# Optimization experiments

Hardware: AMD Instinct MI355X
Metric: run time of the kernel (lower is better)

Reference implementation:

```python
import jax, jax.numpy as jnp
import numpy as np

N = 100000   # nodes
E = 600000   # edges
D = 128      # in_dim == out_dim
ED = 6       # edge_dim
LN_EPS = 1e-5


def setup_inputs() -> dict:
    key = jax.random.key(0)
    ks = jax.random.split(key, 12)
    s = 1.0 / np.sqrt(D)
    se = 1.0 / np.sqrt(ED)
    return {
        "x": jax.random.normal(ks[0], (N, D), dtype=jnp.float32),
        "edge_index": jax.random.randint(ks[1], (2, E), 0, N, dtype=jnp.int64),
        "edge_attr": jax.random.normal(ks[2], (E, ED), dtype=jnp.float32),
        "batch": jnp.zeros((N,), dtype=jnp.int64),
        "W_e": jax.random.uniform(ks[3], (ED, D), jnp.float32, -se, se),
        "b_e": jax.random.uniform(ks[4], (D,), jnp.float32, -se, se),
        "eps": jnp.zeros((), dtype=jnp.float32),  # GINE train_eps init 0
        "W1": jax.random.uniform(ks[5], (D, D), jnp.float32, -s, s),
        "b1": jax.random.uniform(ks[6], (D,), jnp.float32, -s, s),
        "W2": jax.random.uniform(ks[7], (D, D), jnp.float32, -s, s),
        "b2": jax.random.uniform(ks[8], (D,), jnp.float32, -s, s),
        "gamma": jnp.ones((D,), dtype=jnp.float32),
        "beta": jnp.zeros((D,), dtype=jnp.float32),
    }


def reference(x, edge_index, edge_attr, batch, W_e, b_e, eps, W1, b1, W2, b2, gamma, beta):
    src, dst = edge_index[0], edge_index[1]
    # edge embedding: Linear(edge_dim -> in_dim)
    edge_emb = edge_attr @ W_e + b_e                      # [E, D]
    # GINEConv message: ReLU(x_j + edge_emb), scatter-add to target nodes
    msg = jax.nn.relu(x[src] + edge_emb)                  # [E, D]
    agg = jax.ops.segment_sum(msg, dst, num_segments=N)   # [N, D]
    h = (1.0 + eps) * x + agg                             # [N, D]
    # GINE nn: Linear -> ReLU -> Linear
    h = jax.nn.relu(h @ W1 + b1) @ W2 + b2                # [N, D]
    # LayerNorm over feature dim
    mu = jnp.mean(h, axis=-1, keepdims=True)
    var = jnp.var(h, axis=-1, keepdims=True)
    h = (h - mu) * jax.lax.rsqrt(var + LN_EPS) * gamma + beta
    # activation=True -> ReLU; dropout identity in eval mode
    return jax.nn.relu(h)
```

## Files before the change

### kernel.cpp

```cpp
#include <hip/hip_runtime.h>
#include <stdint.h>

#define NN 100000
#define EE 600000
#define DD 128

typedef _Float16 half8 __attribute__((ext_vector_type(8)));
typedef _Float16 h2 __attribute__((ext_vector_type(2)));
typedef float f32x4 __attribute__((ext_vector_type(4)));

static __device__ __forceinline__ uint32_t pack2(float a, float b) {
    h2 h; h.x = (_Float16)a; h.y = (_Float16)b;
    return __builtin_bit_cast(uint32_t, h);
}
static __device__ __forceinline__ h2 cvt22(float2 f) {
    h2 r; r.x = (_Float16)f.x; r.y = (_Float16)f.y; return r;
}

#define NB_HIST ((EE + 255) / 256)
#define NB_CONV (NN * DD / 4 / 256)
template<bool CONV>
__global__ __launch_bounds__(256)
void setup_kernel(const int* __restrict__ ei, const float* __restrict__ x,
                  const float* __restrict__ W1, const float* __restrict__ W2,
                  int* __restrict__ counts, uint32_t* __restrict__ xh,
                  _Float16* __restrict__ w1h, _Float16* __restrict__ w2h)
{
    const int nbc = CONV ? NB_CONV : 0;
    const int b = blockIdx.x, tid = threadIdx.x;
    if (b < NB_HIST) {
        int e = b * 256 + tid;
        if (e < EE) atomicAdd(&counts[ei[EE + e]], 1);
    } else if (CONV && b < NB_HIST + nbc) {
        int i = (b - NB_HIST) * 256 + tid;
        float4 v = ((const float4*)x)[i];
        uint2 o; o.x = pack2(v.x, v.y); o.y = pack2(v.z, v.w);
        ((uint2*)xh)[i] = o;
    } else {
        int t = (b - NB_HIST - nbc) * 256 + tid;
        if (t < 2 * DD * DD) {
            int which = t >> 14;
            int idx = t & (DD * DD - 1);
            int k = idx >> 7, d = idx & 127;
            float wv = (which ? W2 : W1)[k * DD + d];
            int kt = k >> 5, kr = k & 31;
            int grp = kr >> 3, j = kr & 7;
            int nt = d >> 4, cc = d & 15;
            int off = ((kt * 8 + nt) * 64 + grp * 16 + cc) * 8 + j;
            (which ? w2h : w1h)[off] = (_Float16)wv;
        }
    }
}

__global__ __launch_bounds__(256)
void scan_blocks(const int* __restrict__ counts, int* __restrict__ startv,
                 int* __restrict__ bsum)
{
    const int t = threadIdx.x;
    const int idx = blockIdx.x * 1024 + t * 4;
    int4 v = {0, 0, 0, 0};
    if (idx < NN) v = *(const int4*)(counts + idx);
    int s1 = v.x + v.y, s2 = s1 + v.z, s3 = s2 + v.w;
    const int lane = t & 63;
    int q = s3;
#pragma unroll
    for (int off = 1; off < 64; off <<= 1) {
        int u = __shfl_up(q, off, 64);
        if (lane >= off) q += u;
    }
    __shared__ int wsum[4];
    if (lane == 63) wsum[t >> 6] = q;
    __syncthreads();
    const int w = t >> 6;
    int pre = 0;
    if (w > 0) pre += wsum[0];
    if (w > 1) pre += wsum[1];
    if (w > 2) pre += wsum[2];
    const int excl = (q - s3) + pre;
    if (idx < NN) {
        int4 o = {excl, excl + v.x, excl + s1, excl + s2};
        *(int4*)(startv + idx) = o;
    }
    __syncthreads();
    if (t == 0) bsum[blockIdx.x] = wsum[0] + wsum[1] + wsum[2] + wsum[3];
}

__global__ __launch_bounds__(128)
void scan_top(const int* __restrict__ bsum, int* __restrict__ boff)
{
    __shared__ int sm[128];
    const int t = threadIdx.x;
    const int NB = (NN + 1023) / 1024;
    int v = (t < NB) ? bsum[t] : 0;
    sm[t] = v;
    __syncthreads();
#pragma unroll
    for (int off = 1; off < 128; off <<= 1) {
        int u = (t >= off) ? sm[t - off] : 0;
        __syncthreads();
        sm[t] += u;
        __syncthreads();
    }
    boff[t] = sm[t] - v;
}

__global__ __launch_bounds__(256)
void fixup_start(int* __restrict__ start, const int* __restrict__ boff)
{
    int i = blockIdx.x * 256 + threadIdx.x;
    if (i < NN) start[i] += boff[i >> 10];
    if (i == 0) start[NN] = EE;
}

__global__ __launch_bounds__(256)
void scatter_rec(const int* __restrict__ ei, const float* __restrict__ ea,
                 const int* __restrict__ start, int* __restrict__ cursor,
                 float* __restrict__ rec)
{
    int e = blockIdx.x * 256 + threadIdx.x;
    if (e >= EE) return;
    int dst = ei[EE + e];
    int src = ei[e];
    int pos = start[dst] + atomicAdd(&cursor[dst], 1);
    const float2* eap = (const float2*)(ea + e * 6);
    float2 e01 = eap[0];
    float2 e23 = eap[1];
    float2 e45 = eap[2];
    float4 r;
    r.x = __int_as_float(src);
    r.y = __uint_as_float(pack2(e01.x, e01.y));
    r.z = __uint_as_float(pack2(e23.x, e23.y));
    r.w = __uint_as_float(pack2(e45.x, e45.y));
    *(float4*)(rec + (size_t)pos * 4) = r;
}

#define NWAVE 8192
template<bool XH>
__global__ __launch_bounds__(256)
void agg_pk(const float* __restrict__ x, const uint32_t* __restrict__ xh,
            const float* __restrict__ rec, const float* __restrict__ We,
            const float* __restrict__ be, const int* __restrict__ start,
            const float* __restrict__ epsp, uint32_t* __restrict__ h0h)
{
    const int w = blockIdx.x * 4 + (threadIdx.x >> 6);
    const int lane = threadIdx.x & 63;
    const int d0 = lane * 2;
    const h2 w0h = cvt22(*(const float2*)(We + 0 * DD + d0));
    const h2 w1h = cvt22(*(const float2*)(We + 1 * DD + d0));
    const h2 w2h = cvt22(*(const float2*)(We + 2 * DD + d0));
    const h2 w3h = cvt22(*(const float2*)(We + 3 * DD + d0));
    const h2 w4h = cvt22(*(const float2*)(We + 4 * DD + d0));
    const h2 w5h = cvt22(*(const float2*)(We + 5 * DD + d0));
    const h2 bbh = cvt22(*(const float2*)(be + d0));
    h2 zero2; zero2.x = (_Float16)0.f; zero2.y = (_Float16)0.f;
    const float sc = 1.0f + epsp[0];
    const int n0 = (int)(((long long)w * NN) >> 13);
    const int n1 = (int)(((long long)(w + 1) * NN) >> 13);

#define EDGE_PK(R, XV, WGT) do {                                                \
        h2 c01 = __builtin_bit_cast(h2, (R).y);                                 \
        h2 c23 = __builtin_bit_cast(h2, (R).z);                                 \
        h2 c45 = __builtin_bit_cast(h2, (R).w);                                 \
        h2 emb = bbh, s;                                                        \
        s.x = c01.x; s.y = c01.x; emb = s * w0h + emb;                          \
        s.x = c01.y; s.y = c01.y; emb = s * w1h + emb;                          \
        s.x = c23.x; s.y = c23.x; emb = s * w2h + emb;                          \
        s.x = c23.y; s.y = c23.y; emb = s * w3h + emb;                          \
        s.x = c45.x; s.y = c45.x; emb = s * w4h + emb;                          \
        s.x = c45.y; s.y = c45.y; emb = s * w5h + emb;                          \
        h2 m = (XV) + emb;                                                      \
        m = __builtin_elementwise_max(m, zero2);                                \
        ax = fmaf((WGT), (float)m.x, ax);                                       \
        ay = fmaf((WGT), (float)m.y, ay);                                       \
    } while (0)

    for (int n = n0; n < n1; ++n) {
        const int begin = start[n];
        const int cnt = start[n + 1] - begin;
        const float4* rp = (const float4*)rec + begin;
        float ax = 0.f, ay = 0.f;
        for (int i = 0; i < cnt; i += 4) {
            const int rem = cnt - i;
            const int ia = i;
            const int ib = i + (rem > 1 ? 1 : 0);
            const int ic = i + (rem > 2 ? 2 : 0);
            const int id = i + (rem > 3 ? 3 : 0);
            float4 ra = rp[ia], rb = rp[ib], rc = rp[ic], rd = rp[id];
            int sa = __float_as_int(ra.x), sb = __float_as_int(rb.x),
                sc3 = __float_as_int(rc.x), sd = __float_as_int(rd.x);
            h2 xa, xb, xc, xd;
            if constexpr (XH) {
                xa = __builtin_bit_cast(h2, xh[((uint32_t)sa << 6) + lane]);
                xb = __builtin_bit_cast(h2, xh[((uint32_t)sb << 6) + lane]);
                xc = __builtin_bit_cast(h2, xh[((uint32_t)sc3 << 6) + lane]);
                xd = __builtin_bit_cast(h2, xh[((uint32_t)sd << 6) + lane]);
            } else {
                xa = cvt22(*(const float2*)(x + (size_t)sa * DD + d0));
                xb = cvt22(*(const float2*)(x + (size_t)sb * DD + d0));
                xc = cvt22(*(const float2*)(x + (size_t)sc3 * DD + d0));
                xd = cvt22(*(const float2*)(x + (size_t)sd * DD + d0));
            }
            const float wb = rem > 1 ? 1.f : 0.f;
            const float wc = rem > 2 ? 1.f : 0.f;
            const float wd = rem > 3 ? 1.f : 0.f;
            EDGE_PK(ra, xa, 1.f);
            EDGE_PK(rb, xb, wb);
            EDGE_PK(rc, xc, wc);
            EDGE_PK(rd, xd, wd);
        }
        float2 xn = *(const float2*)(x + (size_t)n * DD + d0);
        h0h[(size_t)n * 64 + lane] = pack2(sc * xn.x + ax, sc * xn.y + ay);
    }
#undef EDGE_PK
}

__global__ __launch_bounds__(256)
void prep_w(const float* __restrict__ W1, const float* __restrict__ W2,
            _Float16* __restrict__ w1h, _Float16* __restrict__ w2h)
{
    int t = blockIdx.x * 256 + threadIdx.x;
    if (t >= 2 * DD * DD) return;
    int which = t >> 14;
    int idx = t & (DD * DD - 1);
    int k = idx >> 7, d = idx & 127;
    float wv = (which ? W2 : W1)[k * DD + d];
    int kt = k >> 5, kr = k & 31;
    int grp = kr >> 3, j = kr & 7;
    int nt = d >> 4, cc = d & 15;
    int off = ((kt * 8 + nt) * 64 + grp * 16 + cc) * 8 + j;
    (which ? w2h : w1h)[off] = (_Float16)wv;
}

__global__ __launch_bounds__(256)
void edge_kernel(const float* __restrict__ x, const int* __restrict__ ei,
                 const float* __restrict__ ea, const float* __restrict__ We,
                 const float* __restrict__ be, float* agg)
{
    int tid = blockIdx.x * 256 + threadIdx.x;
    int d0 = (tid & 31) * 4;
    float4 w0 = *(const float4*)(We + 0 * DD + d0);
    float4 w1 = *(const float4*)(We + 1 * DD + d0);
    float4 w2 = *(const float4*)(We + 2 * DD + d0);
    float4 w3 = *(const float4*)(We + 3 * DD + d0);
    float4 w4 = *(const float4*)(We + 4 * DD + d0);
    float4 w5 = *(const float4*)(We + 5 * DD + d0);
    float4 bb = *(const float4*)(be + d0);
    int estride = (gridDim.x * 256) >> 5;
    for (int e = tid >> 5; e < EE; e += estride) {
        int src = ei[e];
        int dst = ei[EE + e];
        const float2* eap = (const float2*)(ea + e * 6);
        float2 e01 = eap[0];
        float2 e23 = eap[1];
        float2 e45 = eap[2];
        float4 xj = *(const float4*)(x + (size_t)src * DD + d0);
        float mx = xj.x + bb.x + e01.x*w0.x + e01.y*w1.x + e23.x*w2.x + e23.y*w3.x + e45.x*w4.x + e45.y*w5.x;
        float my = xj.y + bb.y + e01.x*w0.y + e01.y*w1.y + e23.x*w2.y + e23.y*w3.y + e45.x*w4.y + e45.y*w5.y;
        float mz = xj.z + bb.z + e01.x*w0.z + e01.y*w1.z + e23.x*w2.z + e23.y*w3.z + e45.x*w4.z + e45.y*w5.z;
        float mw = xj.w + bb.w + e01.x*w0.w + e01.y*w1.w + e23.x*w2.w + e23.y*w3.w + e45.x*w4.w + e45.y*w5.w;
        float* ap = agg + (size_t)dst * DD + d0;
        atomicAdd(ap + 0, fmaxf(mx, 0.f));
        atomicAdd(ap + 1, fmaxf(my, 0.f));
        atomicAdd(ap + 2, fmaxf(mz, 0.f));
        atomicAdd(ap + 3, fmaxf(mw, 0.f));
    }
}

template<int MODE>
__global__ __launch_bounds__(256)
void node2(const void* __restrict__ h0p, const float* __restrict__ xp,
           const _Float16* __restrict__ w1h, const _Float16* __restrict__ w2h,
           const float* __restrict__ b1, const float* __restrict__ b2,
           const float* __restrict__ gamma, const float* __restrict__ beta,
           const float* __restrict__ epsp, float* __restrict__ out)
{
    __shared__ _Float16 h1buf[4][16 * 128];
    const int wv = threadIdx.x >> 6;
    const int l  = threadIdx.x & 63;
    const int lm = l & 15;
    const int lg = l >> 4;
    const int rbase = blockIdx.x * 128 + wv * 32;

    float gam[8], bet[8];
#pragma unroll
    for (int nt = 0; nt < 8; ++nt) {
        gam[nt] = gamma[nt * 16 + lm];
        bet[nt] = beta[nt * 16 + lm];
    }

    for (int t = 0; t < 2; ++t) {
        const int r0 = rbase + t * 16;
        int arow = r0 + lm;
        if (arow >= NN) arow = NN - 1;

        half8 a1[4];
#pragma unroll
        for (int kt = 0; kt < 4; ++kt) {
            const int kb = kt * 32 + lg * 8;
            if constexpr (MODE == 0) {
                a1[kt] = *(const half8*)((const _Float16*)h0p + (size_t)arow * DD + kb);
            } else {
                const float4* hp = (const float4*)((const float*)h0p + (size_t)arow * DD + kb);
                float4 p0 = hp[0], p1 = hp[1];
                const float scale = 1.0f + epsp[0];
                const float4* xr = (const float4*)(xp + (size_t)arow * DD + kb);
                float4 x0 = xr[0], x1 = xr[1];
                float v[8] = { x0.x*scale+p0.x, x0.y*scale+p0.y, x0.z*scale+p0.z, x0.w*scale+p0.w,
                               x1.x*scale+p1.x, x1.y*scale+p1.y, x1.z*scale+p1.z, x1.w*scale+p1.w };
#pragma unroll
                for (int j = 0; j < 8; ++j) a1[kt][j] = (_Float16)v[j];
            }
        }

        f32x4 acc[8];
#pragma unroll
        for (int nt = 0; nt < 8; ++nt) { acc[nt][0]=0.f; acc[nt][1]=0.f; acc[nt][2]=0.f; acc[nt][3]=0.f; }
#pragma unroll
        for (int kt = 0; kt < 4; ++kt) {
#pragma unroll
            for (int nt = 0; nt < 8; ++nt) {
                half8 bh = *(const half8*)(w1h + ((size_t)((kt * 8 + nt) * 64 + l)) * 8);
                acc[nt] = __builtin_amdgcn_mfma_f32_16x16x32_f16(a1[kt], bh, acc[nt], 0, 0, 0);
            }
        }

        _Float16* hb = h1buf[wv];
#pragma unroll
        for (int nt = 0; nt < 8; ++nt) {
            const int col = nt * 16 + lm;
            const float bias = b1[col];
#pragma unroll
            for (int q = 0; q < 4; ++q) {
                const int row = lg * 4 + q;
                float v1 = fmaxf(acc[nt][q] + bias, 0.f);
                hb[row * 128 + (col ^ ((row & 7) << 4))] = (_Float16)v1;
            }
        }

        half8 a2[4];
        {
            const int sw = (lm & 7) << 4;
            const _Float16* rowp = hb + lm * 128;
#pragma unroll
            for (int kt = 0; kt < 4; ++kt) {
                const int kb = kt * 32 + lg * 8;
                a2[kt] = *(const half8*)(rowp + (kb ^ sw));
            }
        }

        f32x4 acc2[8];
#pragma unroll
        for (int nt = 0; nt < 8; ++nt) { acc2[nt][0]=0.f; acc2[nt][1]=0.f; acc2[nt][2]=0.f; acc2[nt][3]=0.f; }
#pragma unroll
        for (int kt = 0; kt < 4; ++kt) {
#pragma unroll
            for (int nt = 0; nt < 8; ++nt) {
                half8 bh = *(const half8*)(w2h + ((size_t)((kt * 8 + nt) * 64 + l)) * 8);
                acc2[nt] = __builtin_amdgcn_mfma_f32_16x16x32_f16(a2[kt], bh, acc2[nt], 0, 0, 0);
            }
        }

        float vv[8][4];
        float sums[4] = {0,0,0,0}, sqs[4] = {0,0,0,0};
#pragma unroll
        for (int nt = 0; nt < 8; ++nt) {
            const int col = nt * 16 + lm;
            const float bias = b2[col];
#pragma unroll
            for (int q = 0; q < 4; ++q) {
                float v2 = acc2[nt][q] + bias;
                vv[nt][q] = v2;
                sums[q] += v2;
                sqs[q]  += v2 * v2;
            }
        }
#pragma unroll
        for (int m = 1; m < 16; m <<= 1) {
#pragma unroll
            for (int q = 0; q < 4; ++q) {
                sums[q] += __shfl_xor(sums[q], m, 64);
                sqs[q]  += __shfl_xor(sqs[q],  m, 64);
            }
        }
#pragma unroll
        for (int q = 0; q < 4; ++q) {
            const int grow = r0 + lg * 4 + q;
            if (grow < NN) {
                const float mu  = sums[q] * (1.f / 128.f);
                const float var = sqs[q] * (1.f / 128.f) - mu * mu;
                const float rs  = rsqrtf(var + 1e-5f);
#pragma unroll
                for (int nt = 0; nt < 8; ++nt) {
                    out[(size_t)grow * DD + nt * 16 + lm] =
                        fmaxf((vv[nt][q] - mu) * rs * gam[nt] + bet[nt], 0.f);
                }
            }
        }
    }
}

extern "C" void kernel_launch(void* const* d_in, const int* in_sizes, int n_in,
                              void* d_out, int out_size, void* d_ws, size_t ws_size,
                              hipStream_t stream) {
    (void)in_sizes; (void)n_in; (void)out_size;
    const float* x     = (const float*)d_in[0];
    const int*   ei    = (const int*)d_in[1];
    const float* ea    = (const float*)d_in[2];
    const float* We    = (const float*)d_in[4];
    const float* be    = (const float*)d_in[5];
    const float* epsp  = (const float*)d_in[6];
    const float* W1    = (const float*)d_in[7];
    const float* b1    = (const float*)d_in[8];
    const float* W2    = (const float*)d_in[9];
    const float* b2    = (const float*)d_in[10];
    const float* gamma = (const float*)d_in[11];
    const float* beta  = (const float*)d_in[12];
    float* out = (float*)d_out;

    char* ws = (char*)d_ws;
    _Float16* w1h = (_Float16*)ws;
    _Float16* w2h = w1h + DD * DD;
    size_t off = 2 * (size_t)DD * DD * sizeof(_Float16);
    int* counts = (int*)(ws + off);   off += (size_t)NN * 4;
    int* cursor = (int*)(ws + off);   off += (size_t)NN * 4;
    int* start  = (int*)(ws + off);   off += ((size_t)NN + 1) * 4;
    off = (off + 15) & ~(size_t)15;
    int* bsum   = (int*)(ws + off);   off += 512;
    int* boff   = (int*)(ws + off);   off += 512;
    float* rec  = (float*)(ws + off); off += (size_t)EE * 16;
    uint32_t* h0h = (uint32_t*)(ws + off); off += (size_t)NN * DD * 2;
    const size_t need_h0 = off;
    uint32_t* xh  = (uint32_t*)(ws + off); off += (size_t)NN * DD * 2;
    const size_t need_xh = off;

    const int node_blocks = (NN + 127) / 128;
    const int NBLK = (NN + 1023) / 1024;

    if (ws_size >= need_h0) {
        const bool conv = (ws_size >= need_xh);
        hipMemsetAsync(counts, 0, 2 * (size_t)NN * 4, stream);
        if (conv) {
            setup_kernel<true><<<NB_HIST + NB_CONV + 128, 256, 0, stream>>>(
                ei, x, W1, W2, counts, xh, w1h, w2h);
        } else {
            setup_kernel<false><<<NB_HIST + 128, 256, 0, stream>>>(
                ei, x, W1, W2, counts, xh, w1h, w2h);
        }
        scan_blocks<<<NBLK, 256, 0, stream>>>(counts, start, bsum);
        scan_top<<<1, 128, 0, stream>>>(bsum, boff);
        fixup_start<<<(NN + 255) / 256, 256, 0, stream>>>(start, boff);
        scatter_rec<<<(EE + 255) / 256, 256, 0, stream>>>(ei, ea, start, cursor, rec);
        if (conv) {
            agg_pk<true><<<NWAVE / 4, 256, 0, stream>>>(x, xh, rec, We, be, start, epsp, h0h);
        } else {
            agg_pk<false><<<NWAVE / 4, 256, 0, stream>>>(x, xh, rec, We, be, start, epsp, h0h);
        }
        node2<0><<<node_blocks, 256, 0, stream>>>(h0h, x, w1h, w2h, b1, b2,
                                                  gamma, beta, epsp, out);
    } else {
        hipMemsetAsync(d_out, 0, (size_t)NN * DD * sizeof(float), stream);
        prep_w<<<(2 * DD * DD + 255) / 256, 256, 0, stream>>>(W1, W2, w1h, w2h);
        edge_kernel<<<2048, 256, 0, stream>>>(x, ei, ea, We, be, out);
        node2<2><<<node_blocks, 256, 0, stream>>>(out, x, w1h, w2h, b1, b2,
                                                  gamma, beta, epsp, out);
    }
}
```

Measured before the change: 167.9 us.

## Split wave into 4 edge groups with 16-byte gathers and drop fixup kernel

The main aggregation kernel now splits each wave into four 16-lane groups. Each group handles a different edge of the same node and each lane loads 8 fp16 features with one uint4 gather, and the partial sums are combined with cross-lane shuffles. The fixup_start kernel is removed: consumers add the block offset (boff) to start themselves and read counts directly, which saves one launch. The per-lane register use rises (6x4 weight vectors plus 8 accumulators), and nodes with few edges leave group lanes idle.

```diff
diff --git a/kernel.cpp b/kernel.cpp
--- a/kernel.cpp
+++ b/kernel.cpp
@@ -16,6 +16,8 @@
 static __device__ __forceinline__ h2 cvt22(float2 f) {
     h2 r; r.x = (_Float16)f.x; r.y = (_Float16)f.y; return r;
 }
+static __device__ __forceinline__ h2 bc_lo(h2 v) { h2 r; r.x = v.x; r.y = v.x; return r; }
+static __device__ __forceinline__ h2 bc_hi(h2 v) { h2 r; r.x = v.y; r.y = v.y; return r; }
 
 #define NB_HIST ((EE + 255) / 256)
 #define NB_CONV (NN * DD / 4 / 256)
@@ -105,23 +107,15 @@
 }
 
 __global__ __launch_bounds__(256)
-void fixup_start(int* __restrict__ start, const int* __restrict__ boff)
-{
-    int i = blockIdx.x * 256 + threadIdx.x;
-    if (i < NN) start[i] += boff[i >> 10];
-    if (i == 0) start[NN] = EE;
-}
-
-__global__ __launch_bounds__(256)
 void scatter_rec(const int* __restrict__ ei, const float* __restrict__ ea,
-                 const int* __restrict__ start, int* __restrict__ cursor,
-                 float* __restrict__ rec)
+                 const int* __restrict__ start, const int* __restrict__ boff,
+                 int* __restrict__ cursor, float* __restrict__ rec)
 {
     int e = blockIdx.x * 256 + threadIdx.x;
     if (e >= EE) return;
     int dst = ei[EE + e];
     int src = ei[e];
-    int pos = start[dst] + atomicAdd(&cursor[dst], 1);
+    int pos = start[dst] + boff[dst >> 10] + atomicAdd(&cursor[dst], 1);
     const float2* eap = (const float2*)(ea + e * 6);
     float2 e01 = eap[0];
     float2 e23 = eap[1];
@@ -135,12 +129,95 @@
 }
 
 #define NWAVE 8192
-template<bool XH>
-__global__ __launch_bounds__(256)
-void agg_pk(const float* __restrict__ x, const uint32_t* __restrict__ xh,
-            const float* __restrict__ rec, const float* __restrict__ We,
-            const float* __restrict__ be, const int* __restrict__ start,
-            const float* __restrict__ epsp, uint32_t* __restrict__ h0h)
+__global__ __launch_bounds__(256)
+void agg_g16(const float* __restrict__ x, const uint4* __restrict__ xh4,
+             const float* __restrict__ rec, const float* __restrict__ We,
+             const float* __restrict__ be, const int* __restrict__ start,
+             const int* __restrict__ boff, const int* __restrict__ counts,
+             const float* __restrict__ epsp, uint4* __restrict__ h0h4)
+{
+    const int w = blockIdx.x * 4 + (threadIdx.x >> 6);
+    const int lane = threadIdx.x & 63;
+    const int g  = lane >> 4;
+    const int gl = lane & 15;
+    const int d0 = gl * 8;
+
+    h2 wr[6][4], bb[4];
+#pragma unroll
+    for (int r = 0; r < 6; ++r)
+#pragma unroll
+        for (int p = 0; p < 4; ++p)
+            wr[r][p] = cvt22(*(const float2*)(We + r * DD + d0 + p * 2));
+#pragma unroll
+    for (int p = 0; p < 4; ++p) bb[p] = cvt22(*(const float2*)(be + d0 + p * 2));
+    h2 zero2; zero2.x = (_Float16)0.f; zero2.y = (_Float16)0.f;
+    const float sc = 1.0f + epsp[0];
+    const int n0 = (int)(((long long)w * NN) >> 13);
+    const int n1 = (int)(((long long)(w + 1) * NN) >> 13);
+
+    for (int n = n0; n < n1; ++n) {
+        const int begin = start[n] + boff[n >> 10];
+        const int cnt = counts[n];
+        float acc[8];
+#pragma unroll
+        for (int j = 0; j < 8; ++j) acc[j] = 0.f;
+
+        const int nit = (cnt + 3) >> 2;
+        for (int it = 0; it < nit; ++it) {
+            const int i = it * 4 + g;
+            const float wgt = (i < cnt) ? 1.f : 0.f;
+            const int ic = (i < cnt) ? i : cnt - 1;
+            float4 r = ((const float4*)rec)[begin + ic];
+            const int src = __float_as_int(r.x);
+            uint4 xv = xh4[(size_t)src * 16 + gl];
+            h2 c01 = __builtin_bit_cast(h2, r.y);
+            h2 c23 = __builtin_bit_cast(h2, r.z);
+            h2 c45 = __builtin_bit_cast(h2, r.w);
+            h2 s0 = bc_lo(c01), s1 = bc_hi(c01);
+            h2 s2 = bc_lo(c23), s3 = bc_hi(c23);
+            h2 s4 = bc_lo(c45), s5 = bc_hi(c45);
+            uint32_t xu[4] = {xv.x, xv.y, xv.z, xv.w};
+#pragma unroll
+            for (int p = 0; p < 4; ++p) {
+                h2 m = bb[p];
+                m = s0 * wr[0][p] + m;
+                m = s1 * wr[1][p] + m;
+                m = s2 * wr[2][p] + m;
+                m = s3 * wr[3][p] + m;
+                m = s4 * wr[4][p] + m;
+                m = s5 * wr[5][p] + m;
+                m = m + __builtin_bit_cast(h2, xu[p]);
+                m = __builtin_elementwise_max(m, zero2);
+                acc[2 * p]     = fmaf(wgt, (float)m.x, acc[2 * p]);
+                acc[2 * p + 1] = fmaf(wgt, (float)m.y, acc[2 * p + 1]);
+            }
+        }
+
+#pragma unroll
+        for (int j = 0; j < 8; ++j) {
+            acc[j] += __shfl_xor(acc[j], 16, 64);
+            acc[j] += __shfl_xor(acc[j], 32, 64);
+        }
+
+        if (g == 0) {
+            const float4* xr = (const float4*)(x + (size_t)n * DD + d0);
+            float4 xa = xr[0], xb = xr[1];
+            uint4 u;
+            u.x = pack2(fmaf(sc, xa.x, acc[0]), fmaf(sc, xa.y, acc[1]));
+            u.y = pack2(fmaf(sc, xa.z, acc[2]), fmaf(sc, xa.w, acc[3]));
+            u.z = pack2(fmaf(sc, xb.x, acc[4]), fmaf(sc, xb.y, acc[5]));
+            u.w = pack2(fmaf(sc, xb.z, acc[6]), fmaf(sc, xb.w, acc[7]));
+            h0h4[(size_t)n * 16 + gl] = u;
+        }
+    }
+}
+
+__global__ __launch_bounds__(256)
+void agg_pk(const float* __restrict__ x, const float* __restrict__ rec,
+            const float* __restrict__ We, const float* __restrict__ be,
+            const int* __restrict__ start, const int* __restrict__ boff,
+            const int* __restrict__ counts, const float* __restrict__ epsp,
+            uint32_t* __restrict__ h0h)
 {
     const int w = blockIdx.x * 4 + (threadIdx.x >> 6);
     const int lane = threadIdx.x & 63;
@@ -157,61 +234,32 @@
     const int n0 = (int)(((long long)w * NN) >> 13);
     const int n1 = (int)(((long long)(w + 1) * NN) >> 13);
 
-#define EDGE_PK(R, XV, WGT) do {                                                \
-        h2 c01 = __builtin_bit_cast(h2, (R).y);                                 \
-        h2 c23 = __builtin_bit_cast(h2, (R).z);                                 \
-        h2 c45 = __builtin_bit_cast(h2, (R).w);                                 \
-        h2 emb = bbh, s;                                                        \
-        s.x = c01.x; s.y = c01.x; emb = s * w0h + emb;                          \
-        s.x = c01.y; s.y = c01.y; emb = s * w1h + emb;                          \
-        s.x = c23.x; s.y = c23.x; emb = s * w2h + emb;                          \
-        s.x = c23.y; s.y = c23.y; emb = s * w3h + emb;                          \
-        s.x = c45.x; s.y = c45.x; emb = s * w4h + emb;                          \
-        s.x = c45.y; s.y = c45.y; emb = s * w5h + emb;                          \
-        h2 m = (XV) + emb;                                                      \
-        m = __builtin_elementwise_max(m, zero2);                                \
-        ax = fmaf((WGT), (float)m.x, ax);                                       \
-        ay = fmaf((WGT), (float)m.y, ay);                                       \
-    } while (0)
-
     for (int n = n0; n < n1; ++n) {
-        const int begin = start[n];
-        const int cnt = start[n + 1] - begin;
+        const int begin = start[n] + boff[n >> 10];
+        const int cnt = counts[n];
         const float4* rp = (const float4*)rec + begin;
         float ax = 0.f, ay = 0.f;
-        for (int i = 0; i < cnt; i += 4) {
-            const int rem = cnt - i;
-            const int ia = i;
-            const int ib = i + (rem > 1 ? 1 : 0);
-            const int ic = i + (rem > 2 ? 2 : 0);
-            const int id = i + (rem > 3 ? 3 : 0);
-            float4 ra = rp[ia], rb = rp[ib], rc = rp[ic], rd = rp[id];
-            int sa = __float_as_int(ra.x), sb = __float_as_int(rb.x),
-                sc3 = __float_as_int(rc.x), sd = __float_as_int(rd.x);
-            h2 xa, xb, xc, xd;
-            if constexpr (XH) {
-                xa = __builtin_bit_cast(h2, xh[((uint32_t)sa << 6) + lane]);
-                xb = __builtin_bit_cast(h2, xh[((uint32_t)sb << 6) + lane]);
-                xc = __builtin_bit_cast(h2, xh[((uint32_t)sc3 << 6) + lane]);
-                xd = __builtin_bit_cast(h2, xh[((uint32_t)sd << 6) + lane]);
-            } else {
-                xa = cvt22(*(const float2*)(x + (size_t)sa * DD + d0));
-                xb = cvt22(*(const float2*)(x + (size_t)sb * DD + d0));
-                xc = cvt22(*(const float2*)(x + (size_t)sc3 * DD + d0));
-                xd = cvt22(*(const float2*)(x + (size_t)sd * DD + d0));
-            }
-            const float wb = rem > 1 ? 1.f : 0.f;
-            const float wc = rem > 2 ? 1.f : 0.f;
-            const float wd = rem > 3 ? 1.f : 0.f;
-            EDGE_PK(ra, xa, 1.f);
-            EDGE_PK(rb, xb, wb);
-            EDGE_PK(rc, xc, wc);
-            EDGE_PK(rd, xd, wd);
+        for (int i = 0; i < cnt; ++i) {
+            float4 r = rp[i];
+            int s = __float_as_int(r.x);
+            h2 c01 = __builtin_bit_cast(h2, r.y);
+            h2 c23 = __builtin_bit_cast(h2, r.z);
+            h2 c45 = __builtin_bit_cast(h2, r.w);
+            h2 emb = bbh;
+            emb = bc_lo(c01) * w0h + emb;
+            emb = bc_hi(c01) * w1h + emb;
+            emb = bc_lo(c23) * w2h + emb;
+            emb = bc_hi(c23) * w3h + emb;
+            emb = bc_lo(c45) * w4h + emb;
+            emb = bc_hi(c45) * w5h + emb;
+            h2 m = emb + cvt22(*(const float2*)(x + (size_t)s * DD + d0));
+            m = __builtin_elementwise_max(m, zero2);
+            ax += (float)m.x;
+            ay += (float)m.y;
         }
         float2 xn = *(const float2*)(x + (size_t)n * DD + d0);
-        h0h[(size_t)n * 64 + lane] = pack2(sc * xn.x + ax, sc * xn.y + ay);
-    }
-#undef EDGE_PK
+        h0h[(size_t)n * 64 + lane] = pack2(fmaf(sc, xn.x, ax), fmaf(sc, xn.y, ay));
+    }
 }
 
 __global__ __launch_bounds__(256)
@@ -423,8 +471,7 @@
     size_t off = 2 * (size_t)DD * DD * sizeof(_Float16);
     int* counts = (int*)(ws + off);   off += (size_t)NN * 4;
     int* cursor = (int*)(ws + off);   off += (size_t)NN * 4;
-    int* start  = (int*)(ws + off);   off += ((size_t)NN + 1) * 4;
-    off = (off + 15) & ~(size_t)15;
+    int* start  = (int*)(ws + off);   off += (size_t)NN * 4;
     int* bsum   = (int*)(ws + off);   off += 512;
     int* boff   = (int*)(ws + off);   off += 512;
     float* rec  = (float*)(ws + off); off += (size_t)EE * 16;
@@ -448,12 +495,13 @@
         }
         scan_blocks<<<NBLK, 256, 0, stream>>>(counts, start, bsum);
         scan_top<<<1, 128, 0, stream>>>(bsum, boff);
-        fixup_start<<<(NN + 255) / 256, 256, 0, stream>>>(start, boff);
-        scatter_rec<<<(EE + 255) / 256, 256, 0, stream>>>(ei, ea, start, cursor, rec);
+        scatter_rec<<<(EE + 255) / 256, 256, 0, stream>>>(ei, ea, start, boff, cursor, rec);
         if (conv) {
-            agg_pk<true><<<NWAVE / 4, 256, 0, stream>>>(x, xh, rec, We, be, start, epsp, h0h);
+            agg_g16<<<NWAVE / 4, 256, 0, stream>>>(x, (const uint4*)xh, rec, We, be,
+                                                   start, boff, counts, epsp, (uint4*)h0h);
         } else {
-            agg_pk<false><<<NWAVE / 4, 256, 0, stream>>>(x, xh, rec, We, be, start, epsp, h0h);
+            agg_pk<<<NWAVE / 4, 256, 0, stream>>>(x, rec, We, be, start, boff,
+                                                  counts, epsp, h0h);
         }
         node2<0><<<node_blocks, 256, 0, stream>>>(h0h, x, w1h, w2h, b1, b2,
                                                   gamma, beta, epsp, out);
```

Result: slower. 187.0 us (+11.4%).
